# Optimization experiments

Measured on AMD Instinct MI355X. Metric: run time of the kernel, lower is better.

Reference implementation:

```python
import jax, jax.numpy as jnp
import numpy as np

NUM_EMBEDDINGS = 1024
EMBEDDING_DIM = 256
COMMITMENT_COST = 0.25


def setup_inputs() -> dict:
    key = jax.random.key(0)
    k_z, k_e = jax.random.split(key)
    z = jax.random.normal(k_z, (8, EMBEDDING_DIM, 16, 16, 16), dtype=jnp.float32)
    # nn.Embedding weight initialized uniform(-1/K, 1/K)
    codebook = jax.random.uniform(
        k_e, (NUM_EMBEDDINGS, EMBEDDING_DIM), dtype=jnp.float32,
        minval=-1.0 / NUM_EMBEDDINGS, maxval=1.0 / NUM_EMBEDDINGS)
    return {"z": z, "codebook": codebook}


def reference(z, codebook):
    B, D, H, W, L = z.shape
    # (B, D, H, W, L) -> (B, H, W, L, D) -> (N, D)
    z_perm = jnp.transpose(z, (0, 2, 3, 4, 1))          # (B,H,W,L,D)
    z_flat = z_perm.reshape(-1, D)                       # (N,D)
    # squared-distance via expansion: ||z||^2 + ||e||^2 - 2 z.e^T
    distances = ((z_flat ** 2).sum(axis=1, keepdims=True)
                 + (codebook ** 2).sum(axis=1)
                 - 2.0 * z_flat @ codebook.T)            # (N,K)
    indices = jnp.argmin(distances, axis=1)              # (N,)
    quantized = codebook[indices].reshape(B, H, W, L, D)
    idx_out = indices.reshape(B, H, W, L)
    # losses (stop_gradient mirrors .detach())
    e_latent_loss = jnp.mean((jax.lax.stop_gradient(quantized) - z_perm) ** 2)
    q_latent_loss = jnp.mean((quantized - jax.lax.stop_gradient(z_perm)) ** 2)
    vq_loss = q_latent_loss + COMMITMENT_COST * e_latent_loss
    # straight-through estimator
    quant_st = z_perm + jax.lax.stop_gradient(quantized - z_perm)
    quant_out = jnp.transpose(quant_st, (0, 4, 1, 2, 3))  # (B,D,H,W,L)
    return quant_out, idx_out, vq_loss
```

## Files before the change

### kernel.cpp

```cpp
#include <hip/hip_runtime.h>
#include <hip/hip_bf16.h>


#define K_CODES 1024
#define DIM 256
#define N_TOK 32768
#define SPATIAL 4096
#define TOK_BLK 32
#define CAP 32
#define MARGIN 1e-3f
#define ZPITCH 257

typedef __attribute__((ext_vector_type(8))) short short8;
typedef __attribute__((ext_vector_type(4))) float float4v;

#define WS_LOSS 0
#define WS_DONE_I 1
#define WS_E2 16
#define WS_EB 2048

#define O_IDX (8 * DIM * SPATIAL)
#define O_LOSS (O_IDX + N_TOK)
#define N_BLOCKS (N_TOK / TOK_BLK)

__device__ __forceinline__ short f2bf(float v) {
  unsigned u = __float_as_uint(v);
  u = (u + 0x7fffu + ((u >> 16) & 1u)) >> 16;
  return (short)u;
}

__global__ __launch_bounds__(256) void prep_kernel(const float* __restrict__ e,
                                                   float* __restrict__ ws) {
  int T = blockIdx.x, tid = threadIdx.x;
#pragma unroll
  for (int ii = 0; ii < 2; ii++) {
    int idx = ii * 256 + tid;
    int f = idx >> 6, lane = idx & 63;
    int q = lane >> 4, nn = lane & 15;
    const float* src = e + (size_t)(T * 16 + nn) * DIM + f * 32 + q * 8;
    float4 lo = *(const float4*)src;
    float4 hi = *(const float4*)(src + 4);
    unsigned s0 = (unsigned short)f2bf(lo.x) | ((unsigned)(unsigned short)f2bf(lo.y) << 16);
    unsigned s1 = (unsigned short)f2bf(lo.z) | ((unsigned)(unsigned short)f2bf(lo.w) << 16);
    unsigned s2 = (unsigned short)f2bf(hi.x) | ((unsigned)(unsigned short)f2bf(hi.y) << 16);
    unsigned s3 = (unsigned short)f2bf(hi.z) | ((unsigned)(unsigned short)f2bf(hi.w) << 16);
    uint4 p = {s0, s1, s2, s3};
    ((uint4*)(ws + WS_EB))[(T * 8 + f) * 64 + lane] = p;
  }
  if (tid < 128) {
    int c8 = tid >> 3, slot = tid & 7;
    int k = T * 16 + c8;
    const float* er = e + (size_t)k * DIM;
    float res01[2];
#pragma unroll
    for (int blk = 0; blk < 2; blk++) {
      float v0 = er[blk * 128 + slot];
      float rj = __fmul_rn(v0, v0);
      for (int i = 1; i < 16; i++) {
        float v = er[blk * 128 + i * 8 + slot];
        rj = __fadd_rn(rj, __fmul_rn(v, v));
      }
      float a = __fadd_rn(rj, __shfl_down(rj, 1, 8));
      float bq = __fadd_rn(a, __shfl_down(a, 2, 8));
      res01[blk] = __fadd_rn(bq, __shfl_down(bq, 4, 8));
    }
    if (slot == 0) ws[WS_E2 + k] = __fadd_rn(res01[0], res01[1]);
  }
  if (T == 0 && tid == 0) {
    ws[WS_LOSS] = 0.f;
    ((int*)ws)[WS_DONE_I] = 0;
  }
}

__global__ __launch_bounds__(256, 2) void main_kernel(const float* __restrict__ z,
                                                      const float* __restrict__ e,
                                                      float* __restrict__ ws,
                                                      float* __restrict__ out) {
  __shared__ float zl[TOK_BLK * ZPITCH];
  __shared__ unsigned short cand[TOK_BLK][CAP];
  __shared__ int cnt[TOK_BLK];
  __shared__ float wsmin[4][TOK_BLK];
  __shared__ float thrS[TOK_BLK];
  __shared__ int mini_sh[TOK_BLK];
  __shared__ float red[4];

  int tid = threadIdx.x, w = tid >> 6, lane = tid & 63;
  int quad = lane >> 4, nn = lane & 15;
  int n0 = blockIdx.x * TOK_BLK;
  int b = n0 >> 12, s0 = n0 & 4095;
  const float* zb = z + (size_t)b * DIM * SPATIAL + s0;
  const float* Se = ws + WS_E2;

  if (tid < TOK_BLK) cnt[tid] = 0;

#pragma unroll
  for (int i = 0; i < 8; i++) {
    int idx = i * 256 + tid;
    int d = idx >> 3, g = idx & 7;
    float4 v = *(const float4*)(zb + (size_t)d * SPATIAL + g * 4);
    zl[(4 * g + 0) * ZPITCH + d] = v.x;
    zl[(4 * g + 1) * ZPITCH + d] = v.y;
    zl[(4 * g + 2) * ZPITCH + d] = v.z;
    zl[(4 * g + 3) * ZPITCH + d] = v.w;
  }
  __syncthreads();

  short8 A0[8], A1[8];
#pragma unroll
  for (int f = 0; f < 8; f++) {
    short8 a0, a1;
#pragma unroll
    for (int j = 0; j < 8; j++) {
      int d = f * 32 + quad * 8 + j;
      a0[j] = f2bf(zl[nn * ZPITCH + d]);
      a1[j] = f2bf(zl[(16 + nn) * ZPITCH + d]);
    }
    A0[f] = a0;
    A1[f] = a1;
  }

  const short8* eB8 = (const short8*)(ws + WS_EB);

  float ml0[4] = {3.4e38f, 3.4e38f, 3.4e38f, 3.4e38f};
  float ml1[4] = {3.4e38f, 3.4e38f, 3.4e38f, 3.4e38f};
  for (int c = 0; c < 16; c++) {
    int T = w * 16 + c;
    float4v C0 = {0.f, 0.f, 0.f, 0.f}, C1 = {0.f, 0.f, 0.f, 0.f};
#pragma unroll
    for (int f = 0; f < 8; f++) {
      short8 Bf = eB8[(size_t)(T * 8 + f) * 64 + lane];
      C0 = __builtin_amdgcn_mfma_f32_16x16x32_bf16(A0[f], Bf, C0, 0, 0, 0);
      C1 = __builtin_amdgcn_mfma_f32_16x16x32_bf16(A1[f], Bf, C1, 0, 0, 0);
    }
    float SeK = Se[T * 16 + nn];
#pragma unroll
    for (int r = 0; r < 4; r++) {
      ml0[r] = fminf(ml0[r], fmaf(-2.f, C0[r], SeK));
      ml1[r] = fminf(ml1[r], fmaf(-2.f, C1[r], SeK));
    }
  }
#pragma unroll
  for (int r = 0; r < 4; r++) {
    float m0 = ml0[r], m1 = ml1[r];
    m0 = fminf(m0, __shfl_xor(m0, 1, 16));
    m0 = fminf(m0, __shfl_xor(m0, 2, 16));
    m0 = fminf(m0, __shfl_xor(m0, 4, 16));
    m0 = fminf(m0, __shfl_xor(m0, 8, 16));
    m1 = fminf(m1, __shfl_xor(m1, 1, 16));
    m1 = fminf(m1, __shfl_xor(m1, 2, 16));
    m1 = fminf(m1, __shfl_xor(m1, 4, 16));
    m1 = fminf(m1, __shfl_xor(m1, 8, 16));
    if (nn == 0) {
      wsmin[w][quad * 4 + r] = m0;
      wsmin[w][16 + quad * 4 + r] = m1;
    }
  }
  __syncthreads();
  if (tid < TOK_BLK)
    thrS[tid] = fminf(fminf(wsmin[0][tid], wsmin[1][tid]),
                      fminf(wsmin[2][tid], wsmin[3][tid])) + MARGIN;
  __syncthreads();

  float thr0[4], thr1[4];
#pragma unroll
  for (int r = 0; r < 4; r++) {
    thr0[r] = thrS[quad * 4 + r];
    thr1[r] = thrS[16 + quad * 4 + r];
  }

  for (int c = 0; c < 16; c++) {
    int T = w * 16 + c;
    float4v C0 = {0.f, 0.f, 0.f, 0.f}, C1 = {0.f, 0.f, 0.f, 0.f};
#pragma unroll
    for (int f = 0; f < 8; f++) {
      short8 Bf = eB8[(size_t)(T * 8 + f) * 64 + lane];
      C0 = __builtin_amdgcn_mfma_f32_16x16x32_bf16(A0[f], Bf, C0, 0, 0, 0);
      C1 = __builtin_amdgcn_mfma_f32_16x16x32_bf16(A1[f], Bf, C1, 0, 0, 0);
    }
    float SeK = Se[T * 16 + nn];
    bool p0[4], p1[4];
#pragma unroll
    for (int r = 0; r < 4; r++) {
      p0[r] = fmaf(-2.f, C0[r], SeK) < thr0[r];
      p1[r] = fmaf(-2.f, C1[r], SeK) < thr1[r];
    }
    if (__ballot(p0[0] | p0[1] | p0[2] | p0[3] | p1[0] | p1[1] | p1[2] | p1[3])) {
#pragma unroll
      for (int g = 0; g < 2; g++) {
#pragma unroll
        for (int r = 0; r < 4; r++) {
          bool pr = g ? p1[r] : p0[r];
          unsigned long long bl = __ballot(pr);
          unsigned grp = (unsigned)((bl >> (quad * 16)) & 0xffffULL);
          if (grp) {
            int t = g * 16 + quad * 4 + r;
            int base = 0;
            if (nn == 0) base = atomicAdd(&cnt[t], __popc(grp));
            base = __shfl(base, quad * 16, 64);
            if (pr) {
              int pos = base + __popc(grp & ((1u << nn) - 1u));
              if (pos < CAP) cand[t][pos] = (unsigned short)(T * 16 + nn);
            }
          }
        }
      }
    }
  }
  __syncthreads();

  {
    int t = tid >> 3, slot = tid & 7;
    const float* zt = zl + t * ZPITCH;
    float res01[2];
#pragma unroll
    for (int blk = 0; blk < 2; blk++) {
      float v0 = zt[blk * 128 + slot];
      float rj = __fmul_rn(v0, v0);
      for (int i = 1; i < 16; i++) {
        float v = zt[blk * 128 + i * 8 + slot];
        rj = __fadd_rn(rj, __fmul_rn(v, v));
      }
      float a = __fadd_rn(rj, __shfl_down(rj, 1, 8));
      float bq = __fadd_rn(a, __shfl_down(a, 2, 8));
      res01[blk] = __fadd_rn(bq, __shfl_down(bq, 4, 8));
    }
    float Szn = __fadd_rn(res01[0], res01[1]);
    Szn = __shfl(Szn, lane & ~7, 64);

    int cc = cnt[t];
    float bD = 3.4e38f;
    int bK = 0x7fffffff;
    if (cc <= CAP) {
      for (int c = slot; c < cc; c += 8) {
        int k = cand[t][c];
        const float* er = e + (size_t)k * DIM;
        float acc = 0.f;
        for (int d = 0; d < DIM; d++) acc = fmaf(zt[d], er[d], acc);
        float D = __fsub_rn(__fadd_rn(Szn, Se[k]), __fmul_rn(2.f, acc));
        if (D < bD || (D == bD && k < bK)) { bD = D; bK = k; }
      }
    } else {
      for (int k = slot; k < K_CODES; k += 8) {
        const float* er = e + (size_t)k * DIM;
        float acc = 0.f;
        for (int d = 0; d < DIM; d++) acc = fmaf(zt[d], er[d], acc);
        float D = __fsub_rn(__fadd_rn(Szn, Se[k]), __fmul_rn(2.f, acc));
        if (D < bD || (D == bD && k < bK)) { bD = D; bK = k; }
      }
    }
#pragma unroll
    for (int off = 4; off > 0; off >>= 1) {
      float oD = __shfl_down(bD, off, 8);
      int oK = __shfl_down(bK, off, 8);
      if (oD < bD || (oD == bD && oK < bK)) { bD = oD; bK = oK; }
    }
    if (slot == 0) {
      mini_sh[t] = bK;
      out[O_IDX + n0 + t] = (float)bK;
    }
  }
  __syncthreads();

  float sumsq = 0.f;
  float* op = out + (size_t)b * DIM * SPATIAL + s0;
  for (int i = 0; i < 32; i++) {
    int idx = i * 256 + tid;
    int d = idx >> 5, t2 = idx & 31;
    float v = e[(size_t)mini_sh[t2] * DIM + d];
    float zv = zl[t2 * ZPITCH + d];
    float df = __fsub_rn(v, zv);
    sumsq = fmaf(df, df, sumsq);
    op[(size_t)d * SPATIAL + t2] = v;
  }
#pragma unroll
  for (int o = 32; o > 0; o >>= 1) sumsq += __shfl_down(sumsq, o, 64);
  if (lane == 0) red[w] = sumsq;
  __syncthreads();
  if (tid == 0) {
    atomicAdd(ws + WS_LOSS, red[0] + red[1] + red[2] + red[3]);
    __threadfence();
    int done = atomicAdd((int*)ws + WS_DONE_I, 1);
    if (done == N_BLOCKS - 1) {
      __threadfence();
      float total = atomicAdd(ws + WS_LOSS, 0.f);
      out[O_LOSS] = 1.25f * total / 8388608.f;
    }
  }
}

extern "C" void kernel_launch(void* const* d_in, const int* in_sizes, int n_in,
                              void* d_out, int out_size, void* d_ws, size_t ws_size,
                              hipStream_t stream) {
  const float* z = (const float*)d_in[0];
  const float* e = (const float*)d_in[1];
  float* ws = (float*)d_ws;
  float* out = (float*)d_out;

  prep_kernel<<<K_CODES / 16, 256, 0, stream>>>(e, ws);
  main_kernel<<<N_BLOCKS, 256, 0, stream>>>(z, e, ws, out);
}
```

Measured before the change: 236.8 us.

## Track per-lane top-2 distances to drop the second MFMA candidate pass

The kernel used to run the bf16 MFMA distance sweep twice: once to find the per-token minimum and again to collect candidate codes under the threshold. Now the first sweep keeps each lane's best and second-best score plus the best index. Candidates are then emitted from the best index, and when a lane's second-best also falls under the threshold, all 16 codes that lane covers are added conservatively. This halves the MFMA and codebook-load work, but adds register pressure and may overflow the candidate buffer (CAP) when many near-ties occur.

```diff
diff --git a/kernel.cpp b/kernel.cpp
--- a/kernel.cpp
+++ b/kernel.cpp
@@ -121,8 +121,16 @@
 
   const short8* eB8 = (const short8*)(ws + WS_EB);
 
-  float ml0[4] = {3.4e38f, 3.4e38f, 3.4e38f, 3.4e38f};
-  float ml1[4] = {3.4e38f, 3.4e38f, 3.4e38f, 3.4e38f};
+  float mn1[2][4], mn2[2][4];
+  int ix1[2][4];
+#pragma unroll
+  for (int g = 0; g < 2; g++)
+#pragma unroll
+    for (int r = 0; r < 4; r++) {
+      mn1[g][r] = 3.4e38f;
+      mn2[g][r] = 3.4e38f;
+      ix1[g][r] = w * 256 + nn;
+    }
   for (int c = 0; c < 16; c++) {
     int T = w * 16 + c;
     float4v C0 = {0.f, 0.f, 0.f, 0.f}, C1 = {0.f, 0.f, 0.f, 0.f};
@@ -133,15 +141,22 @@
       C1 = __builtin_amdgcn_mfma_f32_16x16x32_bf16(A1[f], Bf, C1, 0, 0, 0);
     }
     float SeK = Se[T * 16 + nn];
+    int k = T * 16 + nn;
 #pragma unroll
     for (int r = 0; r < 4; r++) {
-      ml0[r] = fminf(ml0[r], fmaf(-2.f, C0[r], SeK));
-      ml1[r] = fminf(ml1[r], fmaf(-2.f, C1[r], SeK));
+      float s0 = fmaf(-2.f, C0[r], SeK);
+      mn2[0][r] = fminf(mn2[0][r], fmaxf(mn1[0][r], s0));
+      ix1[0][r] = (s0 < mn1[0][r]) ? k : ix1[0][r];
+      mn1[0][r] = fminf(mn1[0][r], s0);
+      float s1 = fmaf(-2.f, C1[r], SeK);
+      mn2[1][r] = fminf(mn2[1][r], fmaxf(mn1[1][r], s1));
+      ix1[1][r] = (s1 < mn1[1][r]) ? k : ix1[1][r];
+      mn1[1][r] = fminf(mn1[1][r], s1);
     }
   }
 #pragma unroll
   for (int r = 0; r < 4; r++) {
-    float m0 = ml0[r], m1 = ml1[r];
+    float m0 = mn1[0][r], m1 = mn1[1][r];
     m0 = fminf(m0, __shfl_xor(m0, 1, 16));
     m0 = fminf(m0, __shfl_xor(m0, 2, 16));
     m0 = fminf(m0, __shfl_xor(m0, 4, 16));
@@ -161,47 +176,30 @@
                       fminf(wsmin[2][tid], wsmin[3][tid])) + MARGIN;
   __syncthreads();
 
-  float thr0[4], thr1[4];
-#pragma unroll
-  for (int r = 0; r < 4; r++) {
-    thr0[r] = thrS[quad * 4 + r];
-    thr1[r] = thrS[16 + quad * 4 + r];
-  }
-
-  for (int c = 0; c < 16; c++) {
-    int T = w * 16 + c;
-    float4v C0 = {0.f, 0.f, 0.f, 0.f}, C1 = {0.f, 0.f, 0.f, 0.f};
-#pragma unroll
-    for (int f = 0; f < 8; f++) {
-      short8 Bf = eB8[(size_t)(T * 8 + f) * 64 + lane];
-      C0 = __builtin_amdgcn_mfma_f32_16x16x32_bf16(A0[f], Bf, C0, 0, 0, 0);
-      C1 = __builtin_amdgcn_mfma_f32_16x16x32_bf16(A1[f], Bf, C1, 0, 0, 0);
-    }
-    float SeK = Se[T * 16 + nn];
-    bool p0[4], p1[4];
+#pragma unroll
+  for (int g = 0; g < 2; g++) {
 #pragma unroll
     for (int r = 0; r < 4; r++) {
-      p0[r] = fmaf(-2.f, C0[r], SeK) < thr0[r];
-      p1[r] = fmaf(-2.f, C1[r], SeK) < thr1[r];
-    }
-    if (__ballot(p0[0] | p0[1] | p0[2] | p0[3] | p1[0] | p1[1] | p1[2] | p1[3])) {
-#pragma unroll
-      for (int g = 0; g < 2; g++) {
-#pragma unroll
-        for (int r = 0; r < 4; r++) {
-          bool pr = g ? p1[r] : p0[r];
-          unsigned long long bl = __ballot(pr);
-          unsigned grp = (unsigned)((bl >> (quad * 16)) & 0xffffULL);
-          if (grp) {
-            int t = g * 16 + quad * 4 + r;
-            int base = 0;
-            if (nn == 0) base = atomicAdd(&cnt[t], __popc(grp));
-            base = __shfl(base, quad * 16, 64);
-            if (pr) {
-              int pos = base + __popc(grp & ((1u << nn) - 1u));
-              if (pos < CAP) cand[t][pos] = (unsigned short)(T * 16 + nn);
-            }
-          }
+      int t = g * 16 + quad * 4 + r;
+      float thr = thrS[t];
+      bool p1 = mn1[g][r] < thr;
+      unsigned long long bl = __ballot(p1);
+      unsigned grp = (unsigned)((bl >> (quad * 16)) & 0xffffULL);
+      if (grp) {
+        int base = 0;
+        if (nn == 0) base = atomicAdd(&cnt[t], __popc(grp));
+        base = __shfl(base, quad * 16, 64);
+        if (p1) {
+          int pos = base + __popc(grp & ((1u << nn) - 1u));
+          if (pos < CAP) cand[t][pos] = (unsigned short)ix1[g][r];
+        }
+      }
+      if (mn2[g][r] < thr) {
+        int base2 = atomicAdd(&cnt[t], 16);
+#pragma unroll
+        for (int c2 = 0; c2 < 16; c2++) {
+          int pos = base2 + c2;
+          if (pos < CAP) cand[t][pos] = (unsigned short)((w * 16 + c2) * 16 + nn);
         }
       }
     }
```

Result: slower. 503.0 us (+112.4%).
